# Performance work log

Measured on AMD Instinct MI355X. Metric: run time of the kernel, lower is better.

The kernel has to match this reference:

```python
import jax, jax.numpy as jnp
import numpy as np

# ---- static config (matches torch module defaults) ----
SPATIAL = np.array([[100, 100], [50, 50], [25, 25], [13, 13]], dtype=np.int64)  # [L,2] (H,W)
EMBED, HEADS, LEVELS, POINTS = 256, 8, 4, 4
HEAD_DIM = EMBED // HEADS
TOTAL_POINTS = HEADS * LEVELS * POINTS
BS, LQ = 32, 300
LV = int((SPATIAL[:, 0] * SPATIAL[:, 1]).sum())  # 13294


def setup_inputs() -> dict:
    key = jax.random.key(0)
    ks = jax.random.split(key, 12)
    s = 1.0 / np.sqrt(EMBED)
    return {
        "query": jax.random.normal(ks[0], (BS, LQ, EMBED), jnp.float32),
        "reference_points": jax.random.uniform(ks[1], (BS, LQ, LEVELS, 2), jnp.float32),
        "value": jax.random.normal(ks[2], (BS, LV, EMBED), jnp.float32),
        "value_spatial_shapes": jnp.asarray(SPATIAL),
        # learned parameters (torch: Linear weight [out,in] -> stored here as [in,out])
        "W_off": jax.random.normal(ks[3], (EMBED, TOTAL_POINTS * 2), jnp.float32) * 0.01,
        "b_off": jax.random.normal(ks[4], (TOTAL_POINTS * 2,), jnp.float32) * 0.01,
        "W_attn": jax.random.normal(ks[5], (EMBED, TOTAL_POINTS), jnp.float32) * s,
        "b_attn": jnp.zeros((TOTAL_POINTS,), jnp.float32),
        "W_val": jax.random.normal(ks[6], (EMBED, EMBED), jnp.float32) * s,
        "b_val": jnp.zeros((EMBED,), jnp.float32),
        "W_out": jax.random.normal(ks[7], (EMBED, EMBED), jnp.float32) * s,
        "b_out": jnp.zeros((EMBED,), jnp.float32),
    }


def _bilinear_sample(v, grid, H, W):
    """F.grid_sample(mode='bilinear', padding_mode='zeros', align_corners=False).
    v: [H*W, c], grid: [Lq, P, 2] in [-1, 1] (x, y). Returns [Lq, P, c]."""
    x = (grid[..., 0] + 1.0) * 0.5 * W - 0.5
    y = (grid[..., 1] + 1.0) * 0.5 * H - 0.5
    x0f, y0f = jnp.floor(x), jnp.floor(y)
    lx, ly = x - x0f, y - y0f
    x0, y0 = x0f.astype(jnp.int32), y0f.astype(jnp.int32)

    def gather(iy, ix):
        valid = ((iy >= 0) & (iy < H) & (ix >= 0) & (ix < W)).astype(v.dtype)[..., None]
        idx = jnp.clip(iy, 0, H - 1) * W + jnp.clip(ix, 0, W - 1)
        return v[idx] * valid

    return (gather(y0, x0) * ((1 - ly) * (1 - lx))[..., None]
            + gather(y0, x0 + 1) * ((1 - ly) * lx)[..., None]
            + gather(y0 + 1, x0) * (ly * (1 - lx))[..., None]
            + gather(y0 + 1, x0 + 1) * (ly * lx)[..., None])


def _ms_deform_attn_core(value, sampling_grids, attention_weights):
    """value: [bs, Lv, H, c]; sampling_grids: [bs, Lq, H, L, P, 2] in [-1,1];
    attention_weights: [bs, Lq, H, L, P] -> output [bs, Lq, H*c]."""
    bs, Lq = sampling_grids.shape[:2]
    samples = []
    start = 0
    for lvl in range(LEVELS):
        H, W = int(SPATIAL[lvl, 0]), int(SPATIAL[lvl, 1])
        # [bs, HW, nh, c] -> [bs*nh, HW, c]
        v_l = value[:, start:start + H * W]
        v_l = v_l.transpose(0, 2, 1, 3).reshape(bs * HEADS, H * W, HEAD_DIM)
        # [bs, Lq, nh, P, 2] -> [bs*nh, Lq, P, 2]
        g_l = sampling_grids[:, :, :, lvl].transpose(0, 2, 1, 3, 4).reshape(bs * HEADS, Lq, POINTS, 2)
        samples.append(jax.vmap(lambda vv, gg: _bilinear_sample(vv, gg, H, W))(v_l, g_l))
        start += H * W
    stacked = jnp.stack(samples, axis=2)  # [bs*nh, Lq, L, P, c]
    aw = attention_weights.transpose(0, 2, 1, 3, 4).reshape(bs * HEADS, Lq, LEVELS, POINTS)
    out = (stacked * aw[..., None]).sum(axis=(2, 3))  # [bs*nh, Lq, c]
    return out.reshape(bs, HEADS, Lq, HEAD_DIM).transpose(0, 2, 1, 3).reshape(bs, Lq, EMBED)


def reference(query, reference_points, value, value_spatial_shapes,
              W_off, b_off, W_attn, b_attn, W_val, b_val, W_out, b_out):
    bs, Lq = query.shape[:2]
    Lv = value.shape[1]

    value_p = (value @ W_val + b_val).reshape(bs, Lv, HEADS, HEAD_DIM)

    offsets = (query @ W_off + b_off).reshape(bs, Lq, HEADS, LEVELS, POINTS, 2)
    attn = jax.nn.softmax((query @ W_attn + b_attn).reshape(bs, Lq, HEADS, LEVELS * POINTS), axis=-1)
    attn = attn.reshape(bs, Lq, HEADS, LEVELS, POINTS)

    # offset_normalizer = flip(spatial_shapes) -> (W, H) per level
    norm = jnp.asarray(SPATIAL[:, ::-1].copy(), jnp.float32)  # [L, 2]
    sampling_locations = (reference_points[:, :, None, :, None, :]
                          + offsets / norm[None, None, None, :, None, :])
    sampling_grids = 2.0 * sampling_locations - 1.0

    out = _ms_deform_attn_core(value_p, sampling_grids, attn)
    return out @ W_out + b_out
```

## Files before the change

kernel.cpp:

```cpp
#include <hip/hip_runtime.h>
#include <hip/hip_bf16.h>

#define BS_   32
#define LQ_   300
#define LV_   13294
#define EMBED_ 256
#define HEADS_ 8
#define HEAD_DIM_ 32
#define NCHUNK_ 13294
#define PSTRIDE_ 512

typedef __attribute__((ext_vector_type(8))) short bf16x8;
typedef __attribute__((ext_vector_type(4))) float f32x4;

__device__ inline short f2bf(float f) {
  union { float f; unsigned u; } x; x.f = f;
  return (short)((x.u + 0x7FFF + ((x.u >> 16) & 1)) >> 16);
}
__device__ inline short f2bf_i(float f) {
  union { __hip_bfloat16 h; short s; } u;
  u.h = __float2bfloat16(f);
  return u.s;
}
__device__ inline float bf2f(short s) {
  union { unsigned u; float f; } x; x.u = ((unsigned)(unsigned short)s) << 16;
  return x.f;
}

__device__ __forceinline__ void gld_lds16(const void* g, void* l) {
  __builtin_amdgcn_global_load_lds(
      (const __attribute__((address_space(1))) unsigned int*)g,
      (__attribute__((address_space(3))) unsigned int*)l, 16, 0, 0);
}

__global__ void convert_all(const float* __restrict__ W_off,
                            const float* __restrict__ W_attn,
                            const float* __restrict__ W_val,
                            const float* __restrict__ W_out,
                            short* __restrict__ WtQ,
                            short* __restrict__ WtV,
                            short* __restrict__ WtO) {
  const int n = blockIdx.x;
  const int k = threadIdx.x;
  if (n < 384) {
    WtQ[n * 256 + k] = (n < 256) ? f2bf(W_off[k * 256 + n])
                                 : f2bf(W_attn[k * 128 + (n - 256)]);
  } else if (n < 640) {
    WtV[(n - 384) * 256 + k] = f2bf(W_val[k * 256 + (n - 384)]);
  } else {
    WtO[(n - 640) * 256 + k] = f2bf(W_out[k * 256 + (n - 640)]);
  }
}

__global__ __launch_bounds__(512, 2) void gemm_value_persist(
    const float* __restrict__ A, const short* __restrict__ Wt,
    const float* __restrict__ bias, short* __restrict__ Vp) {
  __shared__ float As[2][32 * 256];

  const int tid = threadIdx.x;
  const int lane = tid & 63;
  const int w = tid >> 6;
  const int lr = lane & 15;
  const int lkq = lane >> 4;

  bf16x8 bfr[2][8];
#pragma unroll
  for (int nf = 0; nf < 2; ++nf) {
    const size_t bbase = (size_t)(w * 32 + nf * 16 + lr) * 256 + lkq * 8;
#pragma unroll
    for (int kt = 0; kt < 8; ++kt)
      bfr[nf][kt] = *(const bf16x8*)(Wt + bbase + kt * 32);
  }
  float bv[2];
#pragma unroll
  for (int nf = 0; nf < 2; ++nf) bv[nf] = bias[w * 32 + nf * 16 + lr];

  auto stage = [&](int buf, int c) {
    const float* src = A + (size_t)c * (32 * 256);
#pragma unroll
    for (int i = 0; i < 4; ++i) {
      const int r = w * 4 + i;
      gld_lds16(src + r * 256 + ((lane ^ (r & 7)) * 4), &As[buf][r * 256]);
    }
  };

  const int c0 = blockIdx.x;
  stage(0, c0);
  asm volatile("s_waitcnt vmcnt(0)" ::: "memory");
  __syncthreads();

  int cb = 0;
  for (int c = c0; c < NCHUNK_; c += PSTRIDE_) {
    const int nxt = c + PSTRIDE_;
    if (nxt < NCHUNK_) stage(cb ^ 1, nxt);

    f32x4 acc[2][2];
#pragma unroll
    for (int i = 0; i < 2; ++i)
#pragma unroll
      for (int jj = 0; jj < 2; ++jj) acc[i][jj] = (f32x4){0.f, 0.f, 0.f, 0.f};

    const float* as = &As[cb][0];
#pragma unroll
    for (int kt = 0; kt < 8; ++kt) {
      const int r0 = lr;
      const int r1 = 16 + lr;
      const int g = kt * 8 + lkq * 2;
      const f32x4 a00 = *(const f32x4*)(as + r0 * 256 + (((g    ) ^ (r0 & 7)) * 4));
      const f32x4 a01 = *(const f32x4*)(as + r0 * 256 + (((g + 1) ^ (r0 & 7)) * 4));
      const f32x4 a10 = *(const f32x4*)(as + r1 * 256 + (((g    ) ^ (r1 & 7)) * 4));
      const f32x4 a11 = *(const f32x4*)(as + r1 * 256 + (((g + 1) ^ (r1 & 7)) * 4));
      bf16x8 af0, af1;
#pragma unroll
      for (int i = 0; i < 4; ++i) {
        af0[i]     = f2bf_i(a00[i]);
        af0[i + 4] = f2bf_i(a01[i]);
        af1[i]     = f2bf_i(a10[i]);
        af1[i + 4] = f2bf_i(a11[i]);
      }
      acc[0][0] = __builtin_amdgcn_mfma_f32_16x16x32_bf16(af0, bfr[0][kt], acc[0][0], 0, 0, 0);
      acc[0][1] = __builtin_amdgcn_mfma_f32_16x16x32_bf16(af0, bfr[1][kt], acc[0][1], 0, 0, 0);
      acc[1][0] = __builtin_amdgcn_mfma_f32_16x16x32_bf16(af1, bfr[0][kt], acc[1][0], 0, 0, 0);
      acc[1][1] = __builtin_amdgcn_mfma_f32_16x16x32_bf16(af1, bfr[1][kt], acc[1][1], 0, 0, 0);
    }

#pragma unroll
    for (int mf = 0; mf < 2; ++mf)
#pragma unroll
      for (int rr = 0; rr < 4; ++rr) {
        const unsigned m = (unsigned)c * 32 + mf * 16 + lkq * 4 + rr;
        const unsigned b_ = m / LV_;
        const unsigned pos = m - b_ * LV_;
        const size_t rowbase = ((size_t)(b_ * HEADS_ + w) * LV_ + pos) * HEAD_DIM_;
#pragma unroll
        for (int nf = 0; nf < 2; ++nf)
          Vp[rowbase + nf * 16 + lr] = f2bf(acc[mf][nf][rr] + bv[nf]);
      }

    if (nxt < NCHUNK_) {
      asm volatile("s_waitcnt vmcnt(16)" ::: "memory");
      asm volatile("s_barrier" ::: "memory");
    }
    cb ^= 1;
  }
}

__global__ __launch_bounds__(384, 2) void gemm_qproj2(
    const float* __restrict__ A, const short* __restrict__ Wt,
    const float* __restrict__ b_off, const float* __restrict__ b_attn,
    float* __restrict__ offs, float* __restrict__ logits) {
  __shared__ float As[64 * 256];

  const int tid = threadIdx.x;
  const int lane = tid & 63;
  const int w = tid >> 6;
  const int n0 = w * 64;
  const size_t m0 = (size_t)blockIdx.x * 64;
  const int lr = lane & 15;
  const int lkq = lane >> 4;

  if (w < 4) {
#pragma unroll
    for (int i = 0; i < 16; ++i) {
      const int row = w * 16 + i;
      gld_lds16(A + (m0 + row) * 256 + ((lane ^ (row & 7)) * 4), As + row * 256);
    }
  }

  bf16x8 bfr[4][8];
#pragma unroll
  for (int nf = 0; nf < 4; ++nf) {
    const size_t bbase = (size_t)(n0 + nf * 16 + lr) * 256 + lkq * 8;
#pragma unroll
    for (int kt = 0; kt < 8; ++kt)
      bfr[nf][kt] = *(const bf16x8*)(Wt + bbase + kt * 32);
  }

  f32x4 acc[4][4];
#pragma unroll
  for (int i = 0; i < 4; ++i)
#pragma unroll
    for (int jj = 0; jj < 4; ++jj) acc[i][jj] = (f32x4){0.f, 0.f, 0.f, 0.f};

  __syncthreads();

#pragma unroll
  for (int kt = 0; kt < 8; ++kt) {
#pragma unroll
    for (int mf = 0; mf < 4; ++mf) {
      const int row = mf * 16 + lr;
      const int gbase = kt * 8 + lkq * 2;
      const f32x4 a0 = *(const f32x4*)(As + row * 256 + ((gbase) ^ (row & 7)) * 4);
      const f32x4 a1 = *(const f32x4*)(As + row * 256 + ((gbase + 1) ^ (row & 7)) * 4);
      bf16x8 af;
#pragma unroll
      for (int i = 0; i < 4; ++i) {
        af[i]     = f2bf_i(a0[i]);
        af[i + 4] = f2bf_i(a1[i]);
      }
#pragma unroll
      for (int nf = 0; nf < 4; ++nf)
        acc[mf][nf] = __builtin_amdgcn_mfma_f32_16x16x32_bf16(af, bfr[nf][kt], acc[mf][nf], 0, 0, 0);
    }
  }

  float bv[4];
#pragma unroll
  for (int nf = 0; nf < 4; ++nf) {
    const int n = n0 + nf * 16 + lr;
    bv[nf] = (n < 256) ? b_off[n] : b_attn[n - 256];
  }
  const int lq4 = lkq * 4;
#pragma unroll
  for (int mf = 0; mf < 4; ++mf)
#pragma unroll
    for (int r = 0; r < 4; ++r) {
      const size_t m = m0 + mf * 16 + lq4 + r;
#pragma unroll
      for (int nf = 0; nf < 4; ++nf) {
        const int n = n0 + nf * 16 + lr;
        if (n < 256) offs[m * 256 + n] = acc[mf][nf][r] + bv[nf];
        else         logits[m * 128 + (n - 256)] = acc[mf][nf][r] + bv[nf];
      }
    }
}

__global__ __launch_bounds__(256, 2) void gemm_qproj(
    const float* __restrict__ A, const short* __restrict__ Wt,
    const float* __restrict__ bias, float* __restrict__ C) {
  __shared__ float As[64 * 256];

  const int tid = threadIdx.x;
  const int lane = tid & 63;
  const int w = tid >> 6;
  const int n0 = w * 64;
  const size_t m0 = (size_t)blockIdx.x * 64;
  const int lr = lane & 15;
  const int lkq = lane >> 4;

#pragma unroll
  for (int i = 0; i < 16; ++i) {
    const int row = w * 16 + i;
    gld_lds16(A + (m0 + row) * 256 + ((lane ^ (row & 7)) * 4), As + row * 256);
  }

  bf16x8 bfr[4][8];
#pragma unroll
  for (int nf = 0; nf < 4; ++nf) {
    const size_t bbase = (size_t)(n0 + nf * 16 + lr) * 256 + lkq * 8;
#pragma unroll
    for (int kt = 0; kt < 8; ++kt)
      bfr[nf][kt] = *(const bf16x8*)(Wt + bbase + kt * 32);
  }

  f32x4 acc[4][4];
#pragma unroll
  for (int i = 0; i < 4; ++i)
#pragma unroll
    for (int jj = 0; jj < 4; ++jj) acc[i][jj] = (f32x4){0.f, 0.f, 0.f, 0.f};

  __syncthreads();

#pragma unroll
  for (int kt = 0; kt < 8; ++kt) {
#pragma unroll
    for (int mf = 0; mf < 4; ++mf) {
      const int row = mf * 16 + lr;
      const int gbase = kt * 8 + lkq * 2;
      const f32x4 a0 = *(const f32x4*)(As + row * 256 + ((gbase) ^ (row & 7)) * 4);
      const f32x4 a1 = *(const f32x4*)(As + row * 256 + ((gbase + 1) ^ (row & 7)) * 4);
      bf16x8 af;
#pragma unroll
      for (int i = 0; i < 4; ++i) {
        af[i]     = f2bf_i(a0[i]);
        af[i + 4] = f2bf_i(a1[i]);
      }
#pragma unroll
      for (int nf = 0; nf < 4; ++nf)
        acc[mf][nf] = __builtin_amdgcn_mfma_f32_16x16x32_bf16(af, bfr[nf][kt], acc[mf][nf], 0, 0, 0);
    }
  }

  float bv[4];
#pragma unroll
  for (int nf = 0; nf < 4; ++nf) bv[nf] = bias[n0 + nf * 16 + lr];
  const int lq4 = lkq * 4;
#pragma unroll
  for (int mf = 0; mf < 4; ++mf)
#pragma unroll
    for (int r = 0; r < 4; ++r) {
      const size_t m = m0 + mf * 16 + lq4 + r;
#pragma unroll
      for (int nf = 0; nf < 4; ++nf) {
        const int n = n0 + nf * 16 + lr;
        C[m * 256 + n] = acc[mf][nf][r] + bv[nf];
      }
    }
}

__global__ __launch_bounds__(256) void msda_sample_fused(
    const float* __restrict__ ref_pts,
    const float* __restrict__ offsets,
    const float* __restrict__ logits,
    const short* __restrict__ value_p,
    float* __restrict__ tmp)
{
  const int t = blockIdx.x * 256 + threadIdx.x;
  const int c8 = t & 3;
  const int h = (t >> 2) & 7;
  const int row = t >> 5;
  const int b = row / LQ_;

  const int HS[4] = {100, 50, 25, 13};
  const int START[4] = {0, 10000, 12500, 13125};

  const float* lg = logits + (size_t)row * 128 + h * 16;
  float wv[16];
  float mx = -1e30f;
#pragma unroll
  for (int i = 0; i < 4; ++i) {
    const f32x4 v = *(const f32x4*)(lg + i * 4);
#pragma unroll
    for (int jj = 0; jj < 4; ++jj) { wv[i * 4 + jj] = v[jj]; mx = fmaxf(mx, v[jj]); }
  }
  float sum = 0.f;
#pragma unroll
  for (int i = 0; i < 16; ++i) { wv[i] = __expf(wv[i] - mx); sum += wv[i]; }
  const float inv = 1.0f / sum;
#pragma unroll
  for (int i = 0; i < 16; ++i) wv[i] *= inv;

  const float* offr = offsets + (size_t)row * 256 + h * 32;
  const float* refr = ref_pts + (size_t)row * 8;

  float acc[8];
#pragma unroll
  for (int jj = 0; jj < 8; ++jj) acc[jj] = 0.f;

#pragma unroll
  for (int l = 0; l < 4; ++l) {
    const int HH = HS[l];
    const int WW = HS[l];
    const float fH = (float)HH, fW = (float)WW;
    const float rx = refr[l * 2 + 0];
    const float ry = refr[l * 2 + 1];
    const short* vbase =
        value_p + ((size_t)(b * HEADS_ + h) * LV_ + START[l]) * HEAD_DIM_ + c8 * 8;
#pragma unroll
    for (int p = 0; p < 4; ++p) {
      const float ox = offr[(l * 4 + p) * 2 + 0];
      const float oy = offr[(l * 4 + p) * 2 + 1];
      const float x = (rx + ox / fW) * fW - 0.5f;
      const float y = (ry + oy / fH) * fH - 0.5f;
      const float x0f = floorf(x), y0f = floorf(y);
      const float fx = x - x0f, fy = y - y0f;
      const int x0 = (int)x0f, y0 = (int)y0f;
      const float wgt = wv[l * 4 + p];
      const float iy0 = (y0 >= 0 && y0 < HH) ? 1.f : 0.f;
      const float iy1 = (y0 + 1 >= 0 && y0 + 1 < HH) ? 1.f : 0.f;
      const float ix0 = (x0 >= 0 && x0 < WW) ? 1.f : 0.f;
      const float ix1 = (x0 + 1 >= 0 && x0 + 1 < WW) ? 1.f : 0.f;
      const float w00 = (1.f - fy) * (1.f - fx) * wgt * iy0 * ix0;
      const float w01 = (1.f - fy) * fx * wgt * iy0 * ix1;
      const float w10 = fy * (1.f - fx) * wgt * iy1 * ix0;
      const float w11 = fy * fx * wgt * iy1 * ix1;
      const int xc0 = min(max(x0, 0), WW - 1);
      const int xc1 = min(max(x0 + 1, 0), WW - 1);
      const int yc0 = min(max(y0, 0), HH - 1);
      const int yc1 = min(max(y0 + 1, 0), HH - 1);
      const bf16x8 q00 = *(const bf16x8*)(vbase + (size_t)(yc0 * WW + xc0) * HEAD_DIM_);
      const bf16x8 q01 = *(const bf16x8*)(vbase + (size_t)(yc0 * WW + xc1) * HEAD_DIM_);
      const bf16x8 q10 = *(const bf16x8*)(vbase + (size_t)(yc1 * WW + xc0) * HEAD_DIM_);
      const bf16x8 q11 = *(const bf16x8*)(vbase + (size_t)(yc1 * WW + xc1) * HEAD_DIM_);
#pragma unroll
      for (int jj = 0; jj < 8; ++jj) {
        acc[jj] += w00 * bf2f(q00[jj]) + w01 * bf2f(q01[jj]) +
                   w10 * bf2f(q10[jj]) + w11 * bf2f(q11[jj]);
      }
    }
  }
  float* o = tmp + (size_t)row * 256 + h * 32 + c8 * 8;
  f32x4 o0 = {acc[0], acc[1], acc[2], acc[3]};
  f32x4 o1 = {acc[4], acc[5], acc[6], acc[7]};
  *(f32x4*)(o) = o0;
  *(f32x4*)(o + 4) = o1;
}

extern "C" void kernel_launch(void* const* d_in, const int* in_sizes, int n_in,
                              void* d_out, int out_size, void* d_ws, size_t ws_size,
                              hipStream_t stream) {
  const float* query  = (const float*)d_in[0];
  const float* refpts = (const float*)d_in[1];
  const float* value  = (const float*)d_in[2];
  const float* W_off  = (const float*)d_in[4];
  const float* b_off  = (const float*)d_in[5];
  const float* W_attn = (const float*)d_in[6];
  const float* b_attn = (const float*)d_in[7];
  const float* W_val  = (const float*)d_in[8];
  const float* b_val  = (const float*)d_in[9];
  const float* W_out  = (const float*)d_in[10];
  const float* b_out  = (const float*)d_in[11];
  float* out = (float*)d_out;

  char* ws = (char*)d_ws;
  short* value_p = (short*)ws;
  size_t off = (size_t)BS_ * HEADS_ * LV_ * HEAD_DIM_ * 2;
  float* offsets = (float*)(ws + off); off += (size_t)BS_ * LQ_ * 256 * 4;
  float* logits  = (float*)(ws + off); off += (size_t)BS_ * LQ_ * 128 * 4;
  float* tmp     = (float*)(ws + off); off += (size_t)BS_ * LQ_ * 256 * 4;
  short* WtQ = (short*)(ws + off); off += 384 * 256 * 2;
  short* WtV = (short*)(ws + off); off += 256 * 256 * 2;
  short* WtO = (short*)(ws + off); off += 256 * 256 * 2;

  const int MQ = BS_ * LQ_;

  convert_all<<<896, 256, 0, stream>>>(W_off, W_attn, W_val, W_out, WtQ, WtV, WtO);
  gemm_qproj2<<<MQ / 64, 384, 0, stream>>>(query, WtQ, b_off, b_attn, offsets, logits);
  gemm_value_persist<<<PSTRIDE_, 512, 0, stream>>>(value, WtV, b_val, value_p);
  msda_sample_fused<<<(MQ * 32) / 256, 256, 0, stream>>>(refpts, offsets, logits, value_p, tmp);
  gemm_qproj<<<MQ / 64, 256, 0, stream>>>(tmp, WtO, b_out, out);
}
```

Measured before the change: 210.8 us.

## Fuse query projection GEMM into persistent value projection kernel

Merges the query offset/attention-logit projection into the persistent value-projection kernel. The first 150 of 512 blocks compute one 64-row query tile each before starting their value chunks, sharing the LDS buffer. This removes one kernel launch and the serialization between the two GEMMs. In exchange, those 150 blocks carry extra work, which can create load imbalance, and the weight fragments are now reloaded per k-step.

```diff
diff --git a/kernel.cpp b/kernel.cpp
--- a/kernel.cpp
+++ b/kernel.cpp
@@ -52,16 +52,85 @@
   }
 }
 
-__global__ __launch_bounds__(512, 2) void gemm_value_persist(
-    const float* __restrict__ A, const short* __restrict__ Wt,
-    const float* __restrict__ bias, short* __restrict__ Vp) {
-  __shared__ float As[2][32 * 256];
+__global__ __launch_bounds__(512, 2) void mega_gemm(
+    const float* __restrict__ value, const short* __restrict__ WtV,
+    const float* __restrict__ b_val, short* __restrict__ Vp,
+    const float* __restrict__ query, const short* __restrict__ WtQ,
+    const float* __restrict__ b_off, const float* __restrict__ b_attn,
+    float* __restrict__ offs, float* __restrict__ logits) {
+  __shared__ float As[16384];
 
   const int tid = threadIdx.x;
   const int lane = tid & 63;
   const int w = tid >> 6;
   const int lr = lane & 15;
   const int lkq = lane >> 4;
+  const int bid = blockIdx.x;
+
+  if (bid < 150) {
+    const size_t m0 = (size_t)bid * 64;
+#pragma unroll
+    for (int i = 0; i < 8; ++i) {
+      const int row = w * 8 + i;
+      gld_lds16(query + (m0 + row) * 256 + ((lane ^ (row & 7)) * 4), As + row * 256);
+    }
+    __syncthreads();
+
+    if (w < 6) {
+      const int n0 = w * 64;
+      f32x4 acc[4][4];
+#pragma unroll
+      for (int i = 0; i < 4; ++i)
+#pragma unroll
+        for (int jj = 0; jj < 4; ++jj) acc[i][jj] = (f32x4){0.f, 0.f, 0.f, 0.f};
+
+#pragma unroll
+      for (int kt = 0; kt < 8; ++kt) {
+        bf16x8 bfr[4];
+#pragma unroll
+        for (int nf = 0; nf < 4; ++nf)
+          bfr[nf] = *(const bf16x8*)(WtQ + (size_t)(n0 + nf * 16 + lr) * 256 + kt * 32 + lkq * 8);
+#pragma unroll
+        for (int mf = 0; mf < 4; ++mf) {
+          const int row = mf * 16 + lr;
+          const int g = kt * 8 + lkq * 2;
+          const f32x4 a0 = *(const f32x4*)(As + row * 256 + (((g    ) ^ (row & 7)) * 4));
+          const f32x4 a1 = *(const f32x4*)(As + row * 256 + (((g + 1) ^ (row & 7)) * 4));
+          bf16x8 af;
+#pragma unroll
+          for (int i = 0; i < 4; ++i) {
+            af[i]     = f2bf_i(a0[i]);
+            af[i + 4] = f2bf_i(a1[i]);
+          }
+#pragma unroll
+          for (int nf = 0; nf < 4; ++nf)
+            acc[mf][nf] = __builtin_amdgcn_mfma_f32_16x16x32_bf16(af, bfr[nf], acc[mf][nf], 0, 0, 0);
+        }
+      }
+
+      float bv[4];
+#pragma unroll
+      for (int nf = 0; nf < 4; ++nf) {
+        const int n = n0 + nf * 16 + lr;
+        bv[nf] = (n < 256) ? b_off[n] : b_attn[n - 256];
+      }
+      const int lq4 = lkq * 4;
+#pragma unroll
+      for (int mf = 0; mf < 4; ++mf)
+#pragma unroll
+        for (int r = 0; r < 4; ++r) {
+          const size_t m = m0 + mf * 16 + lq4 + r;
+#pragma unroll
+          for (int nf = 0; nf < 4; ++nf) {
+            const int n = n0 + nf * 16 + lr;
+            const float v = acc[mf][nf][r] + bv[nf];
+            if (n < 256) offs[m * 256 + n] = v;
+            else         logits[m * 128 + (n - 256)] = v;
+          }
+        }
+    }
+    __syncthreads();
+  }
 
   bf16x8 bfr[2][8];
 #pragma unroll
@@ -69,22 +138,22 @@
     const size_t bbase = (size_t)(w * 32 + nf * 16 + lr) * 256 + lkq * 8;
 #pragma unroll
     for (int kt = 0; kt < 8; ++kt)
-      bfr[nf][kt] = *(const bf16x8*)(Wt + bbase + kt * 32);
+      bfr[nf][kt] = *(const bf16x8*)(WtV + bbase + kt * 32);
   }
   float bv[2];
 #pragma unroll
-  for (int nf = 0; nf < 2; ++nf) bv[nf] = bias[w * 32 + nf * 16 + lr];
+  for (int nf = 0; nf < 2; ++nf) bv[nf] = b_val[w * 32 + nf * 16 + lr];
 
   auto stage = [&](int buf, int c) {
-    const float* src = A + (size_t)c * (32 * 256);
+    const float* src = value + (size_t)c * (32 * 256);
 #pragma unroll
     for (int i = 0; i < 4; ++i) {
       const int r = w * 4 + i;
-      gld_lds16(src + r * 256 + ((lane ^ (r & 7)) * 4), &As[buf][r * 256]);
+      gld_lds16(src + r * 256 + ((lane ^ (r & 7)) * 4), As + buf * 8192 + r * 256);
     }
   };
 
-  const int c0 = blockIdx.x;
+  const int c0 = bid;
   stage(0, c0);
   asm volatile("s_waitcnt vmcnt(0)" ::: "memory");
   __syncthreads();
@@ -100,7 +169,7 @@
 #pragma unroll
       for (int jj = 0; jj < 2; ++jj) acc[i][jj] = (f32x4){0.f, 0.f, 0.f, 0.f};
 
-    const float* as = &As[cb][0];
+    const float* as = As + cb * 8192;
 #pragma unroll
     for (int kt = 0; kt < 8; ++kt) {
       const int r0 = lr;
@@ -143,86 +212,6 @@
     }
     cb ^= 1;
   }
-}
-
-__global__ __launch_bounds__(384, 2) void gemm_qproj2(
-    const float* __restrict__ A, const short* __restrict__ Wt,
-    const float* __restrict__ b_off, const float* __restrict__ b_attn,
-    float* __restrict__ offs, float* __restrict__ logits) {
-  __shared__ float As[64 * 256];
-
-  const int tid = threadIdx.x;
-  const int lane = tid & 63;
-  const int w = tid >> 6;
-  const int n0 = w * 64;
-  const size_t m0 = (size_t)blockIdx.x * 64;
-  const int lr = lane & 15;
-  const int lkq = lane >> 4;
-
-  if (w < 4) {
-#pragma unroll
-    for (int i = 0; i < 16; ++i) {
-      const int row = w * 16 + i;
-      gld_lds16(A + (m0 + row) * 256 + ((lane ^ (row & 7)) * 4), As + row * 256);
-    }
-  }
-
-  bf16x8 bfr[4][8];
-#pragma unroll
-  for (int nf = 0; nf < 4; ++nf) {
-    const size_t bbase = (size_t)(n0 + nf * 16 + lr) * 256 + lkq * 8;
-#pragma unroll
-    for (int kt = 0; kt < 8; ++kt)
-      bfr[nf][kt] = *(const bf16x8*)(Wt + bbase + kt * 32);
-  }
-
-  f32x4 acc[4][4];
-#pragma unroll
-  for (int i = 0; i < 4; ++i)
-#pragma unroll
-    for (int jj = 0; jj < 4; ++jj) acc[i][jj] = (f32x4){0.f, 0.f, 0.f, 0.f};
-
-  __syncthreads();
-
-#pragma unroll
-  for (int kt = 0; kt < 8; ++kt) {
-#pragma unroll
-    for (int mf = 0; mf < 4; ++mf) {
-      const int row = mf * 16 + lr;
-      const int gbase = kt * 8 + lkq * 2;
-      const f32x4 a0 = *(const f32x4*)(As + row * 256 + ((gbase) ^ (row & 7)) * 4);
-      const f32x4 a1 = *(const f32x4*)(As + row * 256 + ((gbase + 1) ^ (row & 7)) * 4);
-      bf16x8 af;
-#pragma unroll
-      for (int i = 0; i < 4; ++i) {
-        af[i]     = f2bf_i(a0[i]);
-        af[i + 4] = f2bf_i(a1[i]);
-      }
-#pragma unroll
-      for (int nf = 0; nf < 4; ++nf)
-        acc[mf][nf] = __builtin_amdgcn_mfma_f32_16x16x32_bf16(af, bfr[nf][kt], acc[mf][nf], 0, 0, 0);
-    }
-  }
-
-  float bv[4];
-#pragma unroll
-  for (int nf = 0; nf < 4; ++nf) {
-    const int n = n0 + nf * 16 + lr;
-    bv[nf] = (n < 256) ? b_off[n] : b_attn[n - 256];
-  }
-  const int lq4 = lkq * 4;
-#pragma unroll
-  for (int mf = 0; mf < 4; ++mf)
-#pragma unroll
-    for (int r = 0; r < 4; ++r) {
-      const size_t m = m0 + mf * 16 + lq4 + r;
-#pragma unroll
-      for (int nf = 0; nf < 4; ++nf) {
-        const int n = n0 + nf * 16 + lr;
-        if (n < 256) offs[m * 256 + n] = acc[mf][nf][r] + bv[nf];
-        else         logits[m * 128 + (n - 256)] = acc[mf][nf][r] + bv[nf];
-      }
-    }
 }
 
 __global__ __launch_bounds__(256, 2) void gemm_qproj(
@@ -415,8 +404,8 @@
   const int MQ = BS_ * LQ_;
 
   convert_all<<<896, 256, 0, stream>>>(W_off, W_attn, W_val, W_out, WtQ, WtV, WtO);
-  gemm_qproj2<<<MQ / 64, 384, 0, stream>>>(query, WtQ, b_off, b_attn, offsets, logits);
-  gemm_value_persist<<<PSTRIDE_, 512, 0, stream>>>(value, WtV, b_val, value_p);
+  mega_gemm<<<PSTRIDE_, 512, 0, stream>>>(value, WtV, b_val, value_p,
+                                          query, WtQ, b_off, b_attn, offsets, logits);
   msda_sample_fused<<<(MQ * 32) / 256, 256, 0, stream>>>(refpts, offsets, logits, value_p, tmp);
   gemm_qproj<<<MQ / 64, 256, 0, stream>>>(tmp, WtO, b_out, out);
 }
```

New measurement: 206.3 us (median of 2 runs). -2.2%, faster.
